# Kernel optimization log

Measured on AMD Instinct MI355X. Metric: run time of the kernel, lower is better.

## Reference

```python
import jax, jax.numpy as jnp
import numpy as np

B, N, F_IN = 256, 256, 128
HID, DEPTH = 48, 4
D_OUT = 97                 # sum(latent_dim [32,32,32,1]) = GraphUNet out_channels
K_SORT = 30
C1, C2, KW2 = 16, 32, 5
POOL_LEN = (K_SORT - 2) // 2 + 1        # 15 after maxpool1d(2,2)
DENSE_DIM = (POOL_LEN - KW2 + 1) * C2   # 352
OUT_DIM = 32


def _gcn(x, A, W, b):
    # GCNConv(improved=True): A_hat = A + 2I; out = D^-1/2 A_hat D^-1/2 (x W) + b
    n = A.shape[-1]
    Ah = A + 2.0 * jnp.eye(n, dtype=A.dtype)
    dinv = jax.lax.rsqrt(jnp.sum(Ah, axis=-1))          # deg >= 2 always
    An = dinv[:, :, None] * Ah * dinv[:, None, :]
    return An @ (x @ W) + b


def _augment(A):
    # GraphUNet.augment_adj: add self loops, two-hop (A@A), remove self loops
    n = A.shape[-1]
    eye = jnp.eye(n, dtype=A.dtype)
    A1 = A + eye
    return (A1 @ A1) * (1.0 - eye)


def _topk_pool(x, A, p):
    # TopKPooling(ratio=0.5, nonlinearity=tanh): score = tanh(x.p/||p||)
    Bb, n, _ = x.shape
    score = jnp.tanh((x @ p) / jnp.sqrt(jnp.sum(p * p)))
    k = (n + 1) // 2
    vals, perm = jax.lax.top_k(score, k)                # [B,k]
    bidx = jnp.arange(Bb)[:, None]
    xp = x[bidx, perm] * vals[..., None]                # gate kept nodes by score
    Ap = A[bidx[..., None], perm[:, :, None], perm[:, None, :]]
    return xp, Ap, perm


def _forward(x, A, dW0, db0, dW, db, pool_p, uW, ub, uWl, ubl, c1W, c1b, c2W, c2b, oW, ob):
    act = jax.nn.relu
    # ---- GraphUNet down path ----
    h = act(_gcn(x, A, dW0, db0))
    xs, As, perms = [h], [A], []
    Acur = A
    for i in range(DEPTH):
        A2 = _augment(Acur)
        h, Acur, perm = _topk_pool(h, A2, pool_p[i])
        h = act(_gcn(h, Acur, dW[i], db[i]))
        if i < DEPTH - 1:
            xs.append(h)
            As.append(Acur)
        perms.append(perm)
    # ---- up path with sum skip connections ----
    for i in range(DEPTH):
        j = DEPTH - 1 - i
        res, Aj, perm = xs[j], As[j], perms[j]
        bidx = jnp.arange(res.shape[0])[:, None]
        up = jnp.zeros_like(res).at[bidx, perm].set(h)
        h = res + up
        if i < DEPTH - 1:
            h = act(_gcn(h, Aj, uW[i], ub[i]))
        else:
            h = _gcn(h, Aj, uWl, ubl)                   # [B,N,D_OUT], no act
    # ---- global_sort_pool: sort nodes by last channel desc, keep top K_SORT ----
    _, order = jax.lax.top_k(h[..., -1], K_SORT)
    sp = h[jnp.arange(B)[:, None], order]               # [B,K_SORT,D_OUT]
    # conv1d(1->C1, kernel=stride=D_OUT) on flattened [B,1,K*D] == per-node linear
    y = jax.nn.relu(jnp.einsum('bkd,cd->bck', sp, c1W) + c1b[None, :, None])  # [B,C1,K]
    y = y.reshape(B, C1, POOL_LEN, 2).max(-1)           # maxpool1d(2,2)
    y = jax.lax.conv_general_dilated(y, c2W, (1,), 'VALID',
                                     dimension_numbers=('NCH', 'OIH', 'NCH'))
    y = jax.nn.relu(y + c2b[None, :, None])             # [B,C2,POOL_LEN-KW2+1]
    return jax.nn.relu(y.reshape(B, -1) @ oW + ob)      # relu(relu(.)) == relu(.)


def setup_inputs():
    key = jax.random.key(0)
    ks = jax.random.split(key, 12)
    x = jax.random.normal(ks[0], (B, N, F_IN), dtype=jnp.float32)
    # symmetric binary adjacency, no self loops, avg degree ~15
    u = jax.random.uniform(ks[1], (B, N, N))
    A = (u < 0.03).astype(jnp.float32)
    A = jnp.maximum(A, A.transpose(0, 2, 1)) * (1.0 - jnp.eye(N, dtype=jnp.float32))
    s = lambda f: np.float32(1.0 / np.sqrt(f))
    return dict(
        x=x, A=A,
        dW0=jax.random.normal(ks[2], (F_IN, HID), dtype=jnp.float32) * s(F_IN),
        db0=jnp.zeros((HID,), jnp.float32),
        dW=jax.random.normal(ks[3], (DEPTH, HID, HID), dtype=jnp.float32) * s(HID),
        db=jnp.zeros((DEPTH, HID), jnp.float32),
        pool_p=jax.random.normal(ks[4], (DEPTH, HID), dtype=jnp.float32) * s(HID),
        uW=jax.random.normal(ks[5], (DEPTH - 1, HID, HID), dtype=jnp.float32) * s(HID),
        ub=jnp.zeros((DEPTH - 1, HID), jnp.float32),
        uWl=jax.random.normal(ks[6], (HID, D_OUT), dtype=jnp.float32) * s(HID),
        ubl=jnp.zeros((D_OUT,), jnp.float32),
        c1W=jax.random.normal(ks[7], (C1, D_OUT), dtype=jnp.float32) * s(D_OUT),
        c1b=jnp.zeros((C1,), jnp.float32),
        c2W=jax.random.normal(ks[8], (C2, C1, KW2), dtype=jnp.float32) * s(C1 * KW2),
        c2b=jnp.zeros((C2,), jnp.float32),
        oW=jax.random.normal(ks[9], (DENSE_DIM, OUT_DIM), dtype=jnp.float32) * s(DENSE_DIM),
        ob=jnp.zeros((OUT_DIM,), jnp.float32),
    )


def reference(x, A, dW0, db0, dW, db, pool_p, uW, ub, uWl, ubl, c1W, c1b, c2W, c2b, oW, ob):
    return _forward(x, A, dW0, db0, dW, db, pool_p, uW, ub, uWl, ubl, c1W, c1b, c2W, c2b, oW, ob)
```

## Files before the change

### kernel.cpp

```cpp
#include <hip/hip_runtime.h>
#include <math.h>

#define BATCH 256
#define NNODE 256
#define FIN   128
#define HID   48
#define DOUT  97

#define WOFF_DW0 0
#define WOFF_DW  6144
#define WOFF_UW  18432
#define WOFF_UWL 27648
#define WTOT     34816

typedef __attribute__((ext_vector_type(8))) short bf16x8_t;
typedef __attribute__((ext_vector_type(4))) float f32x4_t;

__device__ inline unsigned short f2bf(float x) {
  unsigned u = __float_as_uint(x);
  u += 0x7fff + ((u >> 16) & 1);
  return (unsigned short)(u >> 16);
}
__device__ inline float bf2f(unsigned short h) {
  return __uint_as_float(((unsigned)h) << 16);
}

template<int L> __device__ inline float grp_sum(float v) {
  #pragma unroll
  for (int o = L >> 1; o > 0; o >>= 1) v += __shfl_xor(v, o);
  return v;
}
template<int L> __device__ inline int grp_isum(int v) {
  #pragma unroll
  for (int o = L >> 1; o > 0; o >>= 1) v += __shfl_xor(v, o);
  return v;
}

__global__ __launch_bounds__(256) void k_prepA(const float* __restrict__ A,
                                               unsigned short* __restrict__ Abf,
                                               float* __restrict__ dinv, int rows) {
  int wid = (blockIdx.x * 256 + threadIdx.x) >> 6;
  int lane = threadIdx.x & 63;
  if (wid >= rows) return;
  const float4* rp = (const float4*)(A + (size_t)wid * 256);
  float4 v = rp[lane];
  unsigned long long pk = (unsigned long long)f2bf(v.x)
                        | ((unsigned long long)f2bf(v.y) << 16)
                        | ((unsigned long long)f2bf(v.z) << 32)
                        | ((unsigned long long)f2bf(v.w) << 48);
  *(unsigned long long*)(Abf + (size_t)wid * 256 + lane * 4) = pk;
  float s = v.x + v.y + v.z + v.w;
  #pragma unroll
  for (int o = 32; o > 0; o >>= 1) s += __shfl_down(s, o);
  if (lane == 0) dinv[wid] = 1.0f / sqrtf(s + 2.0f);
}

__global__ __launch_bounds__(256) void k_splitW3(const float* __restrict__ dW0,
                                                 const float* __restrict__ dW,
                                                 const float* __restrict__ uW,
                                                 const float* __restrict__ uWl,
                                                 unsigned short* __restrict__ Wp) {
  int idx = blockIdx.x * 256 + threadIdx.x;
  if (idx >= WTOT) return;
  float v;
  if (idx < WOFF_DW) {
    int f = idx / 128, kk = idx - f * 128;
    v = dW0[kk * HID + f];
  } else if (idx < WOFF_UW) {
    int r = idx - WOFF_DW;
    int i = r / 3072; r -= i * 3072;
    int f = r / 64, kk = r - f * 64;
    v = (kk < HID) ? dW[((size_t)i * HID + kk) * HID + f] : 0.f;
  } else if (idx < WOFF_UWL) {
    int r = idx - WOFF_UW;
    int i = r / 3072; r -= i * 3072;
    int f = r / 64, kk = r - f * 64;
    v = (kk < HID) ? uW[((size_t)i * HID + kk) * HID + f] : 0.f;
  } else {
    int r = idx - WOFF_UWL;
    int f = r / 64, kk = r - f * 64;
    v = (f < DOUT && kk < HID) ? uWl[(size_t)kk * DOUT + f] : 0.f;
  }
  unsigned short h = f2bf(v);
  float r1 = v - bf2f(h);
  unsigned short m = f2bf(r1);
  float r2 = r1 - bf2f(m);
  unsigned short l = f2bf(r2);
  Wp[idx] = h;
  Wp[idx + WTOT] = m;
  Wp[idx + 2 * WTOT] = l;
}

template<int KS2>
__global__ __launch_bounds__(256) void k_xws(const float* __restrict__ X,
                                             const unsigned short* __restrict__ Wp,
                                             float* __restrict__ XW,
                                             const float* __restrict__ dinv,
                                             unsigned short* __restrict__ Yth,
                                             unsigned short* __restrict__ Ytl,
                                             int K, int F, int Fpad, int nShift) {
  constexpr int KP = KS2 * 32;
  int mt = (blockIdx.x * 256 + threadIdx.x) >> 6;
  int lane = threadIdx.x & 63;
  int r = lane & 15, q = lane >> 4;
  const float* xr = X + ((long)mt * 16 + r) * K;
  bf16x8_t ah[KS2], am[KS2], al[KS2];
  #pragma unroll
  for (int ks = 0; ks < KS2; ks++) {
    int col0 = ks * 32 + q * 8;
    float v[8];
    if (col0 + 8 <= K) {
      float4 a = *(const float4*)(xr + col0);
      float4 b = *(const float4*)(xr + col0 + 4);
      v[0] = a.x; v[1] = a.y; v[2] = a.z; v[3] = a.w;
      v[4] = b.x; v[5] = b.y; v[6] = b.z; v[7] = b.w;
    } else {
      #pragma unroll
      for (int j = 0; j < 8; j++) v[j] = (col0 + j < K) ? xr[col0 + j] : 0.f;
    }
    #pragma unroll
    for (int j = 0; j < 8; j++) {
      unsigned short h = f2bf(v[j]);
      float r1 = v[j] - bf2f(h);
      unsigned short m = f2bf(r1);
      float r2 = r1 - bf2f(m);
      unsigned short l = f2bf(r2);
      ah[ks][j] = (short)h;
      am[ks][j] = (short)m;
      al[ks][j] = (short)l;
    }
  }
  long row0 = (long)mt * 16 + q * 4;
  float4 dv4 = {0.f, 0.f, 0.f, 0.f};
  long ytBase = 0;
  if (Yth) {
    dv4 = *(const float4*)(dinv + row0);
    int bb = (int)(row0 >> nShift);
    int jj = (int)(row0 & ((1 << nShift) - 1));
    ytBase = (long)bb * Fpad;
    ytBase = ytBase << nShift;
    ytBase += jj;
  }
  int nFT = Fpad >> 4;
  for (int ft = 0; ft < nFT; ft++) {
    int fl = ft * 16 + r;
    const unsigned short* wb = Wp + (size_t)fl * KP + q * 8;
    f32x4_t acc = {0.f, 0.f, 0.f, 0.f};
    #pragma unroll
    for (int ks = 0; ks < KS2; ks++) {
      bf16x8_t bh = *(const bf16x8_t*)(wb + ks * 32);
      bf16x8_t bm = *(const bf16x8_t*)(wb + WTOT + ks * 32);
      bf16x8_t bl = *(const bf16x8_t*)(wb + 2 * WTOT + ks * 32);
      acc = __builtin_amdgcn_mfma_f32_16x16x32_bf16(ah[ks], bh, acc, 0, 0, 0);
      acc = __builtin_amdgcn_mfma_f32_16x16x32_bf16(ah[ks], bm, acc, 0, 0, 0);
      acc = __builtin_amdgcn_mfma_f32_16x16x32_bf16(am[ks], bh, acc, 0, 0, 0);
      acc = __builtin_amdgcn_mfma_f32_16x16x32_bf16(am[ks], bm, acc, 0, 0, 0);
      acc = __builtin_amdgcn_mfma_f32_16x16x32_bf16(ah[ks], bl, acc, 0, 0, 0);
      acc = __builtin_amdgcn_mfma_f32_16x16x32_bf16(al[ks], bh, acc, 0, 0, 0);
    }
    int f = fl;
    if (f < F) {
      if (XW) {
        #pragma unroll
        for (int reg = 0; reg < 4; reg++) XW[(row0 + reg) * F + f] = acc[reg];
      }
      if (Yth) {
        float dvv[4] = {dv4.x, dv4.y, dv4.z, dv4.w};
        unsigned long long hpk = 0, lpk = 0;
        #pragma unroll
        for (int reg = 0; reg < 4; reg++) {
          float v = dvv[reg] * acc[reg];
          unsigned short hi = f2bf(v);
          unsigned short lo = f2bf(v - bf2f(hi));
          hpk |= ((unsigned long long)hi) << (16 * reg);
          lpk |= ((unsigned long long)lo) << (16 * reg);
        }
        long o = ytBase + ((long)f << nShift);
        *(unsigned long long*)(Yth + o) = hpk;
        *(unsigned long long*)(Ytl + o) = lpk;
      }
    }
  }
}

__global__ __launch_bounds__(1024) void k_big(const float* __restrict__ x,
                                              const unsigned short* __restrict__ Wp0,
                                              const unsigned short* __restrict__ Abf0,
                                              const float* __restrict__ D0,
                                              const float* __restrict__ db0,
                                              float* __restrict__ H0) {
  __shared__ __align__(16) char yt0[24576];
  __shared__ __align__(16) char yt1[24576];
  int b = blockIdx.x, t = threadIdx.x;
  int w = t >> 6, lane = t & 63;
  int r = lane & 15, q = lane >> 4;
  const float* Xb = x + (size_t)b * 256 * 128;
  const float* Db = D0 + (size_t)b * 256;
  {
    int m = w;
    const float* xr = Xb + (size_t)(m * 16 + r) * 128;
    bf16x8_t ah[4], am[4], al[4];
    #pragma unroll
    for (int ks = 0; ks < 4; ks++) {
      int col0 = ks * 32 + q * 8;
      float4 a4 = *(const float4*)(xr + col0);
      float4 b4 = *(const float4*)(xr + col0 + 4);
      float v[8] = {a4.x, a4.y, a4.z, a4.w, b4.x, b4.y, b4.z, b4.w};
      #pragma unroll
      for (int j = 0; j < 8; j++) {
        unsigned short h = f2bf(v[j]); float r1 = v[j] - bf2f(h);
        unsigned short mm = f2bf(r1);  float r2 = r1 - bf2f(mm);
        ah[ks][j] = (short)h; am[ks][j] = (short)mm; al[ks][j] = (short)f2bf(r2);
      }
    }
    int row0 = m * 16 + q * 4;
    float4 dv4 = *(const float4*)(Db + row0);
    float dvv[4] = {dv4.x, dv4.y, dv4.z, dv4.w};
    #pragma unroll
    for (int ft = 0; ft < 3; ft++) {
      int fl = ft * 16 + r;
      const unsigned short* wb = Wp0 + (size_t)fl * 128 + q * 8;
      f32x4_t acc = {0.f, 0.f, 0.f, 0.f};
      #pragma unroll
      for (int ks = 0; ks < 4; ks++) {
        bf16x8_t bh = *(const bf16x8_t*)(wb + ks * 32);
        bf16x8_t bm = *(const bf16x8_t*)(wb + WTOT + ks * 32);
        bf16x8_t bl = *(const bf16x8_t*)(wb + 2 * WTOT + ks * 32);
        acc = __builtin_amdgcn_mfma_f32_16x16x32_bf16(ah[ks], bh, acc, 0, 0, 0);
        acc = __builtin_amdgcn_mfma_f32_16x16x32_bf16(ah[ks], bm, acc, 0, 0, 0);
        acc = __builtin_amdgcn_mfma_f32_16x16x32_bf16(am[ks], bh, acc, 0, 0, 0);
        acc = __builtin_amdgcn_mfma_f32_16x16x32_bf16(am[ks], bm, acc, 0, 0, 0);
        acc = __builtin_amdgcn_mfma_f32_16x16x32_bf16(ah[ks], bl, acc, 0, 0, 0);
        acc = __builtin_amdgcn_mfma_f32_16x16x32_bf16(al[ks], bh, acc, 0, 0, 0);
      }
      #pragma unroll
      for (int reg = 0; reg < 4; reg++) {
        float vv = dvv[reg] * acc[reg];
        unsigned short hi = f2bf(vv);
        unsigned short lo = f2bf(vv - bf2f(hi));
        int byte = (fl * 512 + (row0 + reg) * 2) ^ ((fl & 7) << 4);
        *(unsigned short*)(yt0 + byte) = hi;
        *(unsigned short*)(yt1 + byte) = lo;
      }
    }
  }
  __syncthreads();
  {
    int it = w;
    const unsigned short* ap = Abf0 + ((size_t)b * 256 + it * 16 + r) * 256 + q * 8;
    bf16x8_t af[8];
    #pragma unroll
    for (int ks = 0; ks < 8; ks++) af[ks] = *(const bf16x8_t*)(ap + ks * 32);
    #pragma unroll
    for (int ft = 0; ft < 3; ft++) {
      int fl = ft * 16 + r;
      f32x4_t acc = {0.f, 0.f, 0.f, 0.f};
      #pragma unroll
      for (int ks = 0; ks < 8; ks++) {
        int byte = (fl * 512 + (ks * 32 + q * 8) * 2) ^ ((fl & 7) << 4);
        bf16x8_t bh = *(const bf16x8_t*)(yt0 + byte);
        bf16x8_t bl = *(const bf16x8_t*)(yt1 + byte);
        acc = __builtin_amdgcn_mfma_f32_16x16x32_bf16(af[ks], bh, acc, 0, 0, 0);
        acc = __builtin_amdgcn_mfma_f32_16x16x32_bf16(af[ks], bl, acc, 0, 0, 0);
      }
      float bfv = db0[fl];
      #pragma unroll
      for (int reg = 0; reg < 4; reg++) {
        int rr = it * 16 + q * 4 + reg;
        int sbyte = (fl * 512 + rr * 2) ^ ((fl & 7) << 4);
        float selfv = bf2f(*(const unsigned short*)(yt0 + sbyte))
                    + bf2f(*(const unsigned short*)(yt1 + sbyte));
        float d = Db[rr];
        float v = d * acc[reg] + 2.f * d * selfv + bfv;
        H0[((size_t)b * 256 + rr) * 48 + fl] = fmaxf(v, 0.f);
      }
    }
  }
}

template<int MODE>
__device__ inline void gcn128_phase(const float* __restrict__ Xg,
                                    const unsigned short* __restrict__ Wpl,
                                    const unsigned short* __restrict__ A1,
                                    const float* __restrict__ D1b,
                                    const float* __restrict__ bias,
                                    char* yt0, char* yt1,
                                    float* __restrict__ H1,
                                    float* __restrict__ H0b,
                                    const int* sPerm1, int t) {
  int w = t >> 6, lane = t & 63;
  int r = lane & 15, q = lane >> 4;
  for (int task = w; task < 24; task += 16) {
    int m = task / 3, ft = task - m * 3;
    const float* xr = Xg + (size_t)(m * 16 + r) * 48;
    bf16x8_t ah[2], am[2], al[2];
    #pragma unroll
    for (int ks = 0; ks < 2; ks++) {
      int col0 = ks * 32 + q * 8;
      float v[8];
      if (col0 + 8 <= 48) {
        float4 a4 = *(const float4*)(xr + col0);
        float4 b4 = *(const float4*)(xr + col0 + 4);
        v[0]=a4.x; v[1]=a4.y; v[2]=a4.z; v[3]=a4.w;
        v[4]=b4.x; v[5]=b4.y; v[6]=b4.z; v[7]=b4.w;
      } else {
        #pragma unroll
        for (int j = 0; j < 8; j++) v[j] = (col0 + j < 48) ? xr[col0 + j] : 0.f;
      }
      #pragma unroll
      for (int j = 0; j < 8; j++) {
        unsigned short h = f2bf(v[j]); float r1 = v[j] - bf2f(h);
        unsigned short mm = f2bf(r1);  float r2 = r1 - bf2f(mm);
        ah[ks][j] = (short)h; am[ks][j] = (short)mm; al[ks][j] = (short)f2bf(r2);
      }
    }
    int row0 = m * 16 + q * 4;
    float4 dv4 = *(const float4*)(D1b + row0);
    float dvv[4] = {dv4.x, dv4.y, dv4.z, dv4.w};
    int fl = ft * 16 + r;
    const unsigned short* wb = Wpl + (size_t)fl * 64 + q * 8;
    f32x4_t acc = {0.f, 0.f, 0.f, 0.f};
    #pragma unroll
    for (int ks = 0; ks < 2; ks++) {
      bf16x8_t bh = *(const bf16x8_t*)(wb + ks * 32);
      bf16x8_t bm = *(const bf16x8_t*)(wb + WTOT + ks * 32);
      bf16x8_t bl = *(const bf16x8_t*)(wb + 2 * WTOT + ks * 32);
      acc = __builtin_amdgcn_mfma_f32_16x16x32_bf16(ah[ks], bh, acc, 0, 0, 0);
      acc = __builtin_amdgcn_mfma_f32_16x16x32_bf16(ah[ks], bm, acc, 0, 0, 0);
      acc = __builtin_amdgcn_mfma_f32_16x16x32_bf16(am[ks], bh, acc, 0, 0, 0);
      acc = __builtin_amdgcn_mfma_f32_16x16x32_bf16(am[ks], bm, acc, 0, 0, 0);
      acc = __builtin_amdgcn_mfma_f32_16x16x32_bf16(ah[ks], bl, acc, 0, 0, 0);
      acc = __builtin_amdgcn_mfma_f32_16x16x32_bf16(al[ks], bh, acc, 0, 0, 0);
    }
    #pragma unroll
    for (int reg = 0; reg < 4; reg++) {
      float vv = dvv[reg] * acc[reg];
      unsigned short hi = f2bf(vv);
      unsigned short lo = f2bf(vv - bf2f(hi));
      int byte = (fl * 256 + (row0 + reg) * 2) ^ ((fl & 7) << 4);
      *(unsigned short*)(yt0 + byte) = hi;
      *(unsigned short*)(yt1 + byte) = lo;
    }
  }
  __syncthreads();
  for (int task = w; task < 24; task += 16) {
    int it = task / 3, ft = task - it * 3;
    const unsigned short* ap = A1 + (size_t)(it * 16 + r) * 128 + q * 8;
    bf16x8_t af[4];
    #pragma unroll
    for (int ks = 0; ks < 4; ks++) af[ks] = *(const bf16x8_t*)(ap + ks * 32);
    int fl = ft * 16 + r;
    f32x4_t acc = {0.f, 0.f, 0.f, 0.f};
    #pragma unroll
    for (int ks = 0; ks < 4; ks++) {
      int byte = (fl * 256 + (ks * 32 + q * 8) * 2) ^ ((fl & 7) << 4);
      bf16x8_t bh = *(const bf16x8_t*)(yt0 + byte);
      bf16x8_t bl = *(const bf16x8_t*)(yt1 + byte);
      acc = __builtin_amdgcn_mfma_f32_16x16x32_bf16(af[ks], bh, acc, 0, 0, 0);
      acc = __builtin_amdgcn_mfma_f32_16x16x32_bf16(af[ks], bl, acc, 0, 0, 0);
    }
    float bfv = bias[fl];
    #pragma unroll
    for (int reg = 0; reg < 4; reg++) {
      int rr = it * 16 + q * 4 + reg;
      int sbyte = (fl * 256 + rr * 2) ^ ((fl & 7) << 4);
      float selfv = bf2f(*(const unsigned short*)(yt0 + sbyte))
                  + bf2f(*(const unsigned short*)(yt1 + sbyte));
      float d = D1b[rr];
      float v = d * acc[reg] + 2.f * d * selfv + bfv;
      v = fmaxf(v, 0.f);
      if (MODE == 0) H1[(size_t)rr * 48 + fl] = v;
      else {
        int node = sPerm1[rr];
        H0b[(size_t)node * 48 + fl] += v;
      }
    }
  }
  __syncthreads();
}

__device__ inline void xw_dphase(const float* hin, const float* W, const float* dv,
                                 float* xwd, int n, int t) {
  for (int idx = t; idx < n * 48; idx += 1024) {
    int j = idx / 48, f = idx - j * 48;
    const float* hr = hin + j * 48;
    float a = 0.f;
    #pragma unroll
    for (int g = 0; g < 48; g++) a += hr[g] * W[g * 48 + f];
    xwd[idx] = dv[j] * a;
  }
}

__device__ inline void anxw_phase(const float* A, int lda, const float* xwd,
                                  const float* dv, const float* bias,
                                  float* hout, int n, int t) {
  for (int idx = t; idx < n * 48; idx += 1024) {
    int i = idx / 48, f = idx - i * 48;
    const float* ar = A + i * lda;
    float acc = 0.f;
    #pragma unroll 4
    for (int j = 0; j < n; j++) acc += ar[j] * xwd[j * 48 + f];
    float di = dv[i];
    float v = di * acc + 2.f * di * xwd[i * 48 + f] + bias[f];
    hout[idx] = fmaxf(v, 0.f);
  }
}

template<int N, int K>
__device__ inline void pool_phaseT(const float* h, const float* p,
                                   float* sS, int* perm, float* hin, int t) {
  constexpr int LPR = 1024 / N;
  int row = t / LPR, sub = t % LPR;
  float pn = 0.f;
  #pragma unroll
  for (int g = 0; g < 48; g++) pn += p[g] * p[g];
  const float* hr = h + row * 48;
  float acc = 0.f;
  for (int g = sub; g < 48; g += LPR) acc += hr[g] * p[g];
  acc = grp_sum<LPR>(acc);
  if (sub == 0) sS[row] = tanhf(acc / sqrtf(pn));
  __syncthreads();
  {
    float v = sS[row];
    int r = 0;
    for (int j = sub; j < N; j += LPR) {
      float u = sS[j];
      r += (u > v) || (u == v && j < row);
    }
    r = grp_isum<LPR>(r);
    if (sub == 0 && r < K) perm[r] = row;
  }
  __syncthreads();
  for (int idx = t; idx < K * 48; idx += 1024) {
    int r = idx / 48, g = idx - r * 48;
    int pi = perm[r];
    hin[idx] = h[pi * 48 + g] * sS[pi];
  }
  __syncthreads();
}

template<int NN, int KK>
__device__ inline void aug_phaseT(const float* A, int lda, const int* perm,
                                  float* Ao, int ldo, float* dout, int t) {
  for (int idx = t; idx < KK * KK; idx += 1024) {
    int r = idx / KK, c = idx - r * KK;
    int pr = perm[r], pc = perm[c];
    const float* ra = A + pr * lda;
    const float* rc = A + pc * lda;
    float acc = 0.f;
    #pragma unroll 4
    for (int j = 0; j < NN; j++) acc += ra[j] * rc[j];
    float v = acc + 2.f * ra[pc];
    Ao[r * ldo + c] = (r == c) ? 0.f : v;
  }
  __syncthreads();
  {
    constexpr int LPR = 1024 / KK;
    int row = t / LPR, sub = t % LPR;
    float s = 0.f;
    for (int j = sub; j < KK; j += LPR) s += Ao[row * ldo + j];
    s = grp_sum<(LPR > 64 ? 64 : LPR)>(s);
    if (sub == 0) dout[row] = 1.0f / sqrtf(s + 2.0f);
  }
  __syncthreads();
}

__device__ inline void scat_phase(const int* perm, const float* src, float* dst,
                                  int k, int t) {
  for (int idx = t; idx < k * 48; idx += 1024) {
    int r = idx / 48, g = idx - r * 48;
    dst[perm[r] * 48 + g] += src[idx];
  }
  __syncthreads();
}

__global__ __launch_bounds__(1024) void k_mid(const unsigned short* __restrict__ Abf0,
                                              unsigned short* __restrict__ Abf1g,
                                              float* __restrict__ H0,
                                              float* __restrict__ H1g,
                                              float* __restrict__ D1g,
                                              const unsigned short* __restrict__ Wp,
                                              const float* __restrict__ dW,
                                              const float* __restrict__ dbv,
                                              const float* __restrict__ pp,
                                              const float* __restrict__ uW,
                                              const float* __restrict__ ub) {
  int b = blockIdx.x, t = threadIdx.x;
  __shared__ __align__(16) char arena[63488];
  __shared__ int sPerm1[128];
  float* H1 = H1g + (size_t)b * 128 * 48;
  float* H0b = H0 + (size_t)b * 256 * 48;
  unsigned short* A1 = Abf1g + (size_t)b * 128 * 128;
  float* D1b = D1g + (size_t)b * 128;

  {
    float* sc = (float*)arena;
    const float* p = pp;
    float pn = 0.f;
    #pragma unroll
    for (int g = 0; g < 48; g++) pn += p[g] * p[g];
    int row = t >> 2, sub = t & 3;
    const float* hr = H0b + (size_t)row * 48;
    float a = 0.f;
    for (int g = sub; g < 48; g += 4) a += hr[g] * p[g];
    a = grp_sum<4>(a);
    if (!sub) sc[row] = tanhf(a / sqrtf(pn));
    __syncthreads();
    float vv = sc[row];
    int rk = 0;
    for (int j = sub; j < 256; j += 4) {
      float u = sc[j];
      rk += (u > vv) || (u == vv && j < row);
    }
    rk = grp_isum<4>(rk);
    if (!sub && rk < 128) sPerm1[rk] = row;
    __syncthreads();
    for (int idx = t; idx < 128 * 48; idx += 1024) {
      int rr = idx / 48, g = idx - rr * 48;
      int pi = sPerm1[rr];
      H1[idx] = H0b[(size_t)pi * 48 + g] * sc[pi];
    }
  }
  __syncthreads();

  {
    int w = t >> 6, lane = t & 63;
    int r = lane & 15, q = lane >> 4;
    int it = w >> 1, fh = w & 1;
    int rowA = sPerm1[it * 16 + r];
    const unsigned short* Ab = Abf0 + (size_t)b * 256 * 256;
    const unsigned short* pa = Ab + (size_t)rowA * 256 + q * 8;
    bf16x8_t af[8];
    #pragma unroll
    for (int ks = 0; ks < 8; ks++) {
      bf16x8_t a = *(const bf16x8_t*)(pa + ks * 32);
      int da = rowA - ks * 32 - q * 8;
      #pragma unroll
      for (int e = 0; e < 8; e++) if (da == e) a[e] = (short)0x3F80;
      af[ks] = a;
    }
    for (int ft = fh * 4; ft < fh * 4 + 4; ft++) {
      int rowB = sPerm1[ft * 16 + r];
      const unsigned short* pb = Ab + (size_t)rowB * 256 + q * 8;
      f32x4_t acc = {0.f, 0.f, 0.f, 0.f};
      #pragma unroll
      for (int ks = 0; ks < 8; ks++) {
        bf16x8_t bv = *(const bf16x8_t*)(pb + ks * 32);
        int db_ = rowB - ks * 32 - q * 8;
        #pragma unroll
        for (int e = 0; e < 8; e++) if (db_ == e) bv[e] = (short)0x3F80;
        acc = __builtin_amdgcn_mfma_f32_16x16x32_bf16(af[ks], bv, acc, 0, 0, 0);
      }
      int c = ft * 16 + r;
      #pragma unroll
      for (int reg = 0; reg < 4; reg++) {
        int rr = it * 16 + q * 4 + reg;
        float v = (rr == c) ? 0.f : acc[reg];
        A1[(size_t)rr * 128 + c] = f2bf(v);
      }
    }
  }
  __syncthreads();
  {
    int row = t >> 3, sub = t & 7;
    const unsigned* ar = (const unsigned*)(A1 + (size_t)row * 128);
    float s = 0.f;
    for (int jj = sub; jj < 64; jj += 8) {
      unsigned u = ar[jj];
      s += bf2f((unsigned short)(u & 0xffffu)) + bf2f((unsigned short)(u >> 16));
    }
    s = grp_sum<8>(s);
    if (sub == 0) D1b[row] = 1.0f / sqrtf(s + 2.0f);
  }
  __syncthreads();

  gcn128_phase<0>(H1, Wp + WOFF_DW, A1, D1b, dbv,
                  (char*)arena, (char*)arena + 12288, H1, nullptr, sPerm1, t);

  {
    float* sS  = (float*)(arena);
    int*   sP2 = (int*)(arena + 512);
    int*   sP3 = (int*)(arena + 768);
    int*   sP4 = (int*)(arena + 896);
    float* sD2 = (float*)(arena + 960);
    float* sD3 = (float*)(arena + 1216);
    float* sD4 = (float*)(arena + 1344);
    float* sA2 = (float*)(arena + 1536);
    float* sA3 = (float*)(arena + 18176);
    float* sH2 = (float*)(arena + 22400);
    float* sH3 = (float*)(arena + 34688);
    float* sXW = (float*)(arena + 40832);
    float* hin = (float*)(arena + 53120);
    float* sH4 = (float*)(arena + 59264);
    float* sA4 = (float*)(arena + 62336);

    {
      const float* p = pp + 48;
      float pn = 0.f;
      #pragma unroll
      for (int g = 0; g < 48; g++) pn += p[g] * p[g];
      int row = t >> 3, sub = t & 7;
      const float* hr = H1 + (size_t)row * 48;
      float acc = 0.f;
      for (int g = sub; g < 48; g += 8) acc += hr[g] * p[g];
      acc = grp_sum<8>(acc);
      if (sub == 0) sS[row] = tanhf(acc / sqrtf(pn));
      __syncthreads();
      float v = sS[row];
      int rk = 0;
      for (int j = sub; j < 128; j += 8) {
        float u = sS[j];
        rk += (u > v) || (u == v && j < row);
      }
      rk = grp_isum<8>(rk);
      if (sub == 0 && rk < 64) sP2[rk] = row;
      __syncthreads();
    }
    {
      int w = t >> 6, lane = t & 63;
      int r = lane & 15, q = lane >> 4;
      int it = w >> 2, ft = w & 3;
      int rowA = sP2[it * 16 + r];
      int rowB = sP2[ft * 16 + r];
      const unsigned short* pa = A1 + (size_t)rowA * 128 + q * 8;
      const unsigned short* pb = A1 + (size_t)rowB * 128 + q * 8;
      f32x4_t acc = {0.f, 0.f, 0.f, 0.f};
      #pragma unroll
      for (int k0 = 0; k0 < 128; k0 += 32) {
        bf16x8_t a  = *(const bf16x8_t*)(pa + k0);
        bf16x8_t bv = *(const bf16x8_t*)(pb + k0);
        int daA = rowA - k0 - q * 8;
        int daB = rowB - k0 - q * 8;
        #pragma unroll
        for (int e = 0; e < 8; e++) {
          if (daA == e) a[e] = (short)0x3F80;
          if (daB == e) bv[e] = (short)0x3F80;
        }
        acc = __builtin_amdgcn_mfma_f32_16x16x32_bf16(a, bv, acc, 0, 0, 0);
      }
      int c = ft * 16 + r;
      #pragma unroll
      for (int reg = 0; reg < 4; reg++) {
        int rr = it * 16 + q * 4 + reg;
        sA2[rr * 65 + c] = (rr == c) ? 0.f : acc[reg];
      }
    }
    __syncthreads();
    {
      int row = t >> 4, sub = t & 15;
      float s = 0.f;
      for (int j = sub; j < 64; j += 16) s += sA2[row * 65 + j];
      s = grp_sum<16>(s);
      if (sub == 0) sD2[row] = 1.0f / sqrtf(s + 2.0f);
    }
    __syncthreads();
    for (int idx = t; idx < 64 * 48; idx += 1024) {
      int j = idx / 48, f = idx - j * 48;
      int pi = sP2[j];
      const float* hr = H1 + (size_t)pi * 48;
      const float* W = dW + 2304;
      float a = 0.f;
      #pragma unroll
      for (int g = 0; g < 48; g++) a += hr[g] * W[g * 48 + f];
      sXW[idx] = sD2[j] * sS[pi] * a;
    }
    __syncthreads();
    anxw_phase(sA2, 65, sXW, sD2, dbv + 48, sH2, 64, t);
    __syncthreads();

    pool_phaseT<64, 32>(sH2, pp + 96, sS, sP3, hin, t);
    aug_phaseT<64, 32>(sA2, 65, sP3, sA3, 33, sD3, t);
    xw_dphase(hin, dW + 2 * 2304, sD3, sXW, 32, t);
    __syncthreads();
    anxw_phase(sA3, 33, sXW, sD3, dbv + 96, sH3, 32, t);
    __syncthreads();

    pool_phaseT<32, 16>(sH3, pp + 144, sS, sP4, hin, t);
    aug_phaseT<32, 16>(sA3, 33, sP4, sA4, 17, sD4, t);
    xw_dphase(hin, dW + 3 * 2304, sD4, sXW, 16, t);
    __syncthreads();
    anxw_phase(sA4, 17, sXW, sD4, dbv + 144, sH4, 16, t);
    __syncthreads();

    scat_phase(sP4, sH4, sH3, 16, t);
    xw_dphase(sH3, uW, sD3, sXW, 32, t);
    __syncthreads();
    anxw_phase(sA3, 33, sXW, sD3, ub, sH3, 32, t);
    __syncthreads();

    scat_phase(sP3, sH3, sH2, 32, t);
    xw_dphase(sH2, uW + 2304, sD2, sXW, 64, t);
    __syncthreads();
    anxw_phase(sA2, 65, sXW, sD2, ub + 48, sH2, 64, t);
    __syncthreads();

    for (int idx = t; idx < 64 * 48; idx += 1024) {
      int r2 = idx / 48, g = idx - r2 * 48;
      H1[(size_t)sP2[r2] * 48 + g] += sH2[idx];
    }
  }
  __syncthreads();

  gcn128_phase<1>(H1, Wp + WOFF_UW + 2 * 3072, A1, D1b, ub + 96,
                  (char*)arena, (char*)arena + 12288, nullptr, H0b, sPerm1, t);
}

__global__ __launch_bounds__(1024) void k_htail(const unsigned short* __restrict__ Abf,
                                                const float* __restrict__ dinv,
                                                const unsigned short* __restrict__ Yth,
                                                const unsigned short* __restrict__ Ytl,
                                                const float* __restrict__ ubl,
                                                float* __restrict__ sp) {
  int b = blockIdx.x, t = threadIdx.x;
  __shared__ float sy[256];
  __shared__ float sc[256];
  __shared__ int sord[32];
  const unsigned short* yh = Yth + ((size_t)b * 112 + 96) * 256;
  const unsigned short* yl = Ytl + ((size_t)b * 112 + 96) * 256;
  if (t < 256) sy[t] = bf2f(yh[t]) + bf2f(yl[t]);
  __syncthreads();
  {
    int i = t >> 2, sub = t & 3;
    const unsigned short* ar = Abf + ((size_t)b * 256 + i) * 256 + sub * 64;
    const float* syp = sy + sub * 64;
    float s = 0.f;
    for (int j = 0; j < 64; j += 2) {
      unsigned u = *(const unsigned*)(ar + j);
      s += bf2f((unsigned short)(u & 0xffffu)) * syp[j]
         + bf2f((unsigned short)(u >> 16)) * syp[j + 1];
    }
    s = grp_sum<4>(s);
    if (sub == 0) {
      float d = dinv[(size_t)b * 256 + i];
      sc[i] = d * s + 2.f * d * sy[i];
    }
  }
  __syncthreads();
  {
    int i = t >> 2, sub = t & 3;
    float v = sc[i];
    int rk = 0;
    int j0 = sub * 64;
    for (int j = j0; j < j0 + 64; j++) {
      float u = sc[j];
      rk += (u > v) || (u == v && j < i);
    }
    rk = grp_isum<4>(rk);
    if (sub == 0 && rk < 30) sord[rk] = i;
  }
  __syncthreads();
  int w = t >> 6, lane = t & 63;
  if (w < 14) {
    int it = w / 7, ft = w % 7;
    int r = lane & 15, q = lane >> 4;
    int ari = it * 16 + r;
    int arow = sord[ari < 30 ? ari : 0];
    const unsigned short* ap = Abf + ((size_t)b * 256 + arow) * 256 + q * 8;
    bf16x8_t af[8];
    #pragma unroll
    for (int ks = 0; ks < 8; ks++) af[ks] = *(const bf16x8_t*)(ap + ks * 32);
    int fl = ft * 16 + r;
    const unsigned short* yrowh = Yth + ((size_t)b * 112 + fl) * 256;
    const unsigned short* yrowl = Ytl + ((size_t)b * 112 + fl) * 256;
    f32x4_t acc = {0.f, 0.f, 0.f, 0.f};
    #pragma unroll
    for (int ks = 0; ks < 8; ks++) {
      bf16x8_t bh = *(const bf16x8_t*)(yrowh + q * 8 + ks * 32);
      bf16x8_t bl = *(const bf16x8_t*)(yrowl + q * 8 + ks * 32);
      acc = __builtin_amdgcn_mfma_f32_16x16x32_bf16(af[ks], bh, acc, 0, 0, 0);
      acc = __builtin_amdgcn_mfma_f32_16x16x32_bf16(af[ks], bl, acc, 0, 0, 0);
    }
    if (fl < DOUT) {
      float bf = ubl[fl];
      #pragma unroll
      for (int reg = 0; reg < 4; reg++) {
        int rowidx = it * 16 + q * 4 + reg;
        if (rowidx < 30) {
          int node = sord[rowidx];
          float d = dinv[(size_t)b * 256 + node];
          float yv = bf2f(yrowh[node]) + bf2f(yrowl[node]);
          sp[((size_t)b * 30 + rowidx) * DOUT + fl] = d * acc[reg] + 2.f * d * yv + bf;
        }
      }
    }
  }
}

__global__ __launch_bounds__(256) void k_head2(const float* __restrict__ spg,
                                               const float* __restrict__ c1W,
                                               const float* __restrict__ c1b,
                                               const float* __restrict__ c2W,
                                               const float* __restrict__ c2b,
                                               const float* __restrict__ oW,
                                               const float* __restrict__ ob,
                                               float* __restrict__ out) {
  int b = blockIdx.x, t = threadIdx.x;
  __shared__ float sp[30 * 97];
  __shared__ float y1[16 * 30];
  __shared__ float yp[16 * 15];
  __shared__ float yc[32 * 11];
  __shared__ float red[256];
  const float* spb = spg + (size_t)b * 30 * 97;
  for (int idx = t; idx < 30 * 97; idx += 256) sp[idx] = spb[idx];
  __syncthreads();
  for (int idx = t; idx < 16 * 30; idx += 256) {
    int c = idx / 30, kk = idx - c * 30;
    float a = c1b[c];
    for (int d = 0; d < 97; d++) a += sp[kk * 97 + d] * c1W[c * 97 + d];
    y1[c * 30 + kk] = fmaxf(a, 0.f);
  }
  __syncthreads();
  for (int idx = t; idx < 16 * 15; idx += 256) {
    int c = idx / 15, t2 = idx - c * 15;
    yp[idx] = fmaxf(y1[c * 30 + 2 * t2], y1[c * 30 + 2 * t2 + 1]);
  }
  __syncthreads();
  for (int idx = t; idx < 32 * 11; idx += 256) {
    int o = idx / 11, t3 = idx - o * 11;
    float a = c2b[o];
    for (int i2 = 0; i2 < 16; i2++)
      for (int w = 0; w < 5; w++)
        a += yp[i2 * 15 + t3 + w] * c2W[(o * 16 + i2) * 5 + w];
    yc[o * 11 + t3] = fmaxf(a, 0.f);
  }
  __syncthreads();
  {
    int o = t & 31, g = t >> 5;
    float a = 0.f;
    for (int qq = g * 44; qq < g * 44 + 44; qq++) a += yc[qq] * oW[qq * 32 + o];
    red[t] = a;
  }
  __syncthreads();
  if (t < 32) {
    float a = ob[t];
    #pragma unroll
    for (int g = 0; g < 8; g++) a += red[t + 32 * g];
    out[(size_t)b * 32 + t] = fmaxf(a, 0.f);
  }
}

extern "C" void kernel_launch(void* const* d_in, const int* in_sizes, int n_in,
                              void* d_out, int out_size, void* d_ws, size_t ws_size,
                              hipStream_t stream) {
  const float* x   = (const float*)d_in[0];
  const float* A0  = (const float*)d_in[1];
  const float* dW0 = (const float*)d_in[2];
  const float* db0 = (const float*)d_in[3];
  const float* dW  = (const float*)d_in[4];
  const float* dbv = (const float*)d_in[5];
  const float* pp  = (const float*)d_in[6];
  const float* uW  = (const float*)d_in[7];
  const float* ub  = (const float*)d_in[8];
  const float* uWl = (const float*)d_in[9];
  const float* ubl = (const float*)d_in[10];
  const float* c1W = (const float*)d_in[11];
  const float* c1b = (const float*)d_in[12];
  const float* c2W = (const float*)d_in[13];
  const float* c2b = (const float*)d_in[14];
  const float* oW  = (const float*)d_in[15];
  const float* ob  = (const float*)d_in[16];
  float* out = (float*)d_out;

  float* base = (float*)d_ws;
  size_t off = 0;
  auto alloc = [&](size_t nel) { nel = (nel + 3) & ~(size_t)3; float* p = base + off; off += nel; return p; };
  float* H0 = alloc((size_t)BATCH * 256 * HID);
  float* H1 = alloc((size_t)BATCH * 128 * HID);
  float* D0 = alloc((size_t)BATCH * 256);
  float* D1 = alloc((size_t)BATCH * 128);
  float* SP = alloc((size_t)BATCH * 30 * 97);
  unsigned short* Abf0 = (unsigned short*)alloc((size_t)BATCH * 256 * 256 / 2);
  unsigned short* Abf1 = (unsigned short*)alloc((size_t)BATCH * 128 * 128 / 2);
  unsigned short* Yth  = (unsigned short*)alloc((size_t)BATCH * 112 * 256 / 2);
  unsigned short* Ytl  = (unsigned short*)alloc((size_t)BATCH * 112 * 256 / 2);
  unsigned short* Wp   = (unsigned short*)alloc((size_t)3 * WTOT / 2 + 4);

  k_prepA<<<BATCH * 256 / 4, 256, 0, stream>>>(A0, Abf0, D0, BATCH * 256);
  k_splitW3<<<(WTOT + 255) / 256, 256, 0, stream>>>(dW0, dW, uW, uWl, Wp);

  k_big<<<BATCH, 1024, 0, stream>>>(x, Wp + WOFF_DW0, Abf0, D0, db0, H0);

  k_mid<<<BATCH, 1024, 0, stream>>>(Abf0, Abf1, H0, H1, D1, Wp, dW, dbv, pp, uW, ub);

  k_xws<2><<<BATCH * 256 / 64, 256, 0, stream>>>(H0, Wp + WOFF_UWL, nullptr,
                                                 D0, Yth, Ytl, HID, DOUT, 112, 8);
  k_htail<<<BATCH, 1024, 0, stream>>>(Abf0, D0, Yth, Ytl, ubl, SP);

  k_head2<<<BATCH, 256, 0, stream>>>(SP, c1W, c1b, c2W, c2b, oW, ob, out);
}
```

Baseline: 356.0 us.

## Fuse final XW projection into tail kernel and merge pool/augment phases

```diff
diff --git a/kernel.cpp b/kernel.cpp
--- a/kernel.cpp
+++ b/kernel.cpp
@@ -91,98 +91,6 @@
   Wp[idx + 2 * WTOT] = l;
 }
 
-template<int KS2>
-__global__ __launch_bounds__(256) void k_xws(const float* __restrict__ X,
-                                             const unsigned short* __restrict__ Wp,
-                                             float* __restrict__ XW,
-                                             const float* __restrict__ dinv,
-                                             unsigned short* __restrict__ Yth,
-                                             unsigned short* __restrict__ Ytl,
-                                             int K, int F, int Fpad, int nShift) {
-  constexpr int KP = KS2 * 32;
-  int mt = (blockIdx.x * 256 + threadIdx.x) >> 6;
-  int lane = threadIdx.x & 63;
-  int r = lane & 15, q = lane >> 4;
-  const float* xr = X + ((long)mt * 16 + r) * K;
-  bf16x8_t ah[KS2], am[KS2], al[KS2];
-  #pragma unroll
-  for (int ks = 0; ks < KS2; ks++) {
-    int col0 = ks * 32 + q * 8;
-    float v[8];
-    if (col0 + 8 <= K) {
-      float4 a = *(const float4*)(xr + col0);
-      float4 b = *(const float4*)(xr + col0 + 4);
-      v[0] = a.x; v[1] = a.y; v[2] = a.z; v[3] = a.w;
-      v[4] = b.x; v[5] = b.y; v[6] = b.z; v[7] = b.w;
-    } else {
-      #pragma unroll
-      for (int j = 0; j < 8; j++) v[j] = (col0 + j < K) ? xr[col0 + j] : 0.f;
-    }
-    #pragma unroll
-    for (int j = 0; j < 8; j++) {
-      unsigned short h = f2bf(v[j]);
-      float r1 = v[j] - bf2f(h);
-      unsigned short m = f2bf(r1);
-      float r2 = r1 - bf2f(m);
-      unsigned short l = f2bf(r2);
-      ah[ks][j] = (short)h;
-      am[ks][j] = (short)m;
-      al[ks][j] = (short)l;
-    }
-  }
-  long row0 = (long)mt * 16 + q * 4;
-  float4 dv4 = {0.f, 0.f, 0.f, 0.f};
-  long ytBase = 0;
-  if (Yth) {
-    dv4 = *(const float4*)(dinv + row0);
-    int bb = (int)(row0 >> nShift);
-    int jj = (int)(row0 & ((1 << nShift) - 1));
-    ytBase = (long)bb * Fpad;
-    ytBase = ytBase << nShift;
-    ytBase += jj;
-  }
-  int nFT = Fpad >> 4;
-  for (int ft = 0; ft < nFT; ft++) {
-    int fl = ft * 16 + r;
-    const unsigned short* wb = Wp + (size_t)fl * KP + q * 8;
-    f32x4_t acc = {0.f, 0.f, 0.f, 0.f};
-    #pragma unroll
-    for (int ks = 0; ks < KS2; ks++) {
-      bf16x8_t bh = *(const bf16x8_t*)(wb + ks * 32);
-      bf16x8_t bm = *(const bf16x8_t*)(wb + WTOT + ks * 32);
-      bf16x8_t bl = *(const bf16x8_t*)(wb + 2 * WTOT + ks * 32);
-      acc = __builtin_amdgcn_mfma_f32_16x16x32_bf16(ah[ks], bh, acc, 0, 0, 0);
-      acc = __builtin_amdgcn_mfma_f32_16x16x32_bf16(ah[ks], bm, acc, 0, 0, 0);
-      acc = __builtin_amdgcn_mfma_f32_16x16x32_bf16(am[ks], bh, acc, 0, 0, 0);
-      acc = __builtin_amdgcn_mfma_f32_16x16x32_bf16(am[ks], bm, acc, 0, 0, 0);
-      acc = __builtin_amdgcn_mfma_f32_16x16x32_bf16(ah[ks], bl, acc, 0, 0, 0);
-      acc = __builtin_amdgcn_mfma_f32_16x16x32_bf16(al[ks], bh, acc, 0, 0, 0);
-    }
-    int f = fl;
-    if (f < F) {
-      if (XW) {
-        #pragma unroll
-        for (int reg = 0; reg < 4; reg++) XW[(row0 + reg) * F + f] = acc[reg];
-      }
-      if (Yth) {
-        float dvv[4] = {dv4.x, dv4.y, dv4.z, dv4.w};
-        unsigned long long hpk = 0, lpk = 0;
-        #pragma unroll
-        for (int reg = 0; reg < 4; reg++) {
-          float v = dvv[reg] * acc[reg];
-          unsigned short hi = f2bf(v);
-          unsigned short lo = f2bf(v - bf2f(hi));
-          hpk |= ((unsigned long long)hi) << (16 * reg);
-          lpk |= ((unsigned long long)lo) << (16 * reg);
-        }
-        long o = ytBase + ((long)f << nShift);
-        *(unsigned long long*)(Yth + o) = hpk;
-        *(unsigned long long*)(Ytl + o) = lpk;
-      }
-    }
-  }
-}
-
 __global__ __launch_bounds__(1024) void k_big(const float* __restrict__ x,
                                               const unsigned short* __restrict__ Wp0,
                                               const unsigned short* __restrict__ Abf0,
@@ -407,8 +315,11 @@
 }
 
 template<int N, int K>
-__device__ inline void pool_phaseT(const float* h, const float* p,
-                                   float* sS, int* perm, float* hin, int t) {
+__device__ inline void pool_aug_phaseT(const float* h, const float* p,
+                                       const float* A, int lda,
+                                       float* Ao, int ldo,
+                                       float* sS, int* perm, float* hin,
+                                       float* dout, int t) {
   constexpr int LPR = 1024 / N;
   int row = t / LPR, sub = t % LPR;
   float pn = 0.f;
@@ -422,13 +333,13 @@
   __syncthreads();
   {
     float v = sS[row];
-    int r = 0;
+    int rk = 0;
     for (int j = sub; j < N; j += LPR) {
       float u = sS[j];
-      r += (u > v) || (u == v && j < row);
-    }
-    r = grp_isum<LPR>(r);
-    if (sub == 0 && r < K) perm[r] = row;
+      rk += (u > v) || (u == v && j < row);
+    }
+    rk = grp_isum<LPR>(rk);
+    if (sub == 0 && rk < K) perm[rk] = row;
   }
   __syncthreads();
   for (int idx = t; idx < K * 48; idx += 1024) {
@@ -436,31 +347,26 @@
     int pi = perm[r];
     hin[idx] = h[pi * 48 + g] * sS[pi];
   }
-  __syncthreads();
-}
-
-template<int NN, int KK>
-__device__ inline void aug_phaseT(const float* A, int lda, const int* perm,
-                                  float* Ao, int ldo, float* dout, int t) {
-  for (int idx = t; idx < KK * KK; idx += 1024) {
-    int r = idx / KK, c = idx - r * KK;
+  for (int idx = t; idx < K * K; idx += 1024) {
+    int r = idx / K, c = idx - r * K;
     int pr = perm[r], pc = perm[c];
     const float* ra = A + pr * lda;
     const float* rc = A + pc * lda;
-    float acc = 0.f;
+    float a2 = 0.f;
     #pragma unroll 4
-    for (int j = 0; j < NN; j++) acc += ra[j] * rc[j];
-    float v = acc + 2.f * ra[pc];
+    for (int j = 0; j < N; j++) a2 += ra[j] * rc[j];
+    float v = a2 + 2.f * ra[pc];
     Ao[r * ldo + c] = (r == c) ? 0.f : v;
   }
   __syncthreads();
   {
-    constexpr int LPR = 1024 / KK;
-    int row = t / LPR, sub = t % LPR;
+    constexpr int LPR2 = 1024 / K;
+    constexpr int LG = (LPR2 > 64 ? 64 : LPR2);
+    int row2 = t / LPR2, sub2 = t % LPR2;
     float s = 0.f;
-    for (int j = sub; j < KK; j += LPR) s += Ao[row * ldo + j];
-    s = grp_sum<(LPR > 64 ? 64 : LPR)>(s);
-    if (sub == 0) dout[row] = 1.0f / sqrtf(s + 2.0f);
+    for (int j = sub2; j < K; j += LPR2) s += Ao[row2 * ldo + j];
+    s = grp_sum<LG>(s);
+    if (sub2 == 0) dout[row2] = 1.0f / sqrtf(s + 2.0f);
   }
   __syncthreads();
 }
@@ -514,16 +420,16 @@
     }
     rk = grp_isum<4>(rk);
     if (!sub && rk < 128) sPerm1[rk] = row;
-    __syncthreads();
+  }
+  __syncthreads();
+
+  {
+    float* sc = (float*)arena;
     for (int idx = t; idx < 128 * 48; idx += 1024) {
       int rr = idx / 48, g = idx - rr * 48;
       int pi = sPerm1[rr];
       H1[idx] = H0b[(size_t)pi * 48 + g] * sc[pi];
     }
-  }
-  __syncthreads();
-
-  {
     int w = t >> 6, lane = t & 63;
     int r = lane & 15, q = lane >> 4;
     int it = w >> 1, fh = w & 1;
@@ -668,15 +574,13 @@
     anxw_phase(sA2, 65, sXW, sD2, dbv + 48, sH2, 64, t);
     __syncthreads();
 
-    pool_phaseT<64, 32>(sH2, pp + 96, sS, sP3, hin, t);
-    aug_phaseT<64, 32>(sA2, 65, sP3, sA3, 33, sD3, t);
+    pool_aug_phaseT<64, 32>(sH2, pp + 96, sA2, 65, sA3, 33, sS, sP3, hin, sD3, t);
     xw_dphase(hin, dW + 2 * 2304, sD3, sXW, 32, t);
     __syncthreads();
     anxw_phase(sA3, 33, sXW, sD3, dbv + 96, sH3, 32, t);
     __syncthreads();
 
-    pool_phaseT<32, 16>(sH3, pp + 144, sS, sP4, hin, t);
-    aug_phaseT<32, 16>(sA3, 33, sP4, sA4, 17, sD4, t);
+    pool_aug_phaseT<32, 16>(sH3, pp + 144, sA3, 33, sA4, 17, sS, sP4, hin, sD4, t);
     xw_dphase(hin, dW + 3 * 2304, sD4, sXW, 16, t);
     __syncthreads();
     anxw_phase(sA4, 17, sXW, sD4, dbv + 144, sH4, 16, t);
@@ -705,34 +609,108 @@
                   (char*)arena, (char*)arena + 12288, nullptr, H0b, sPerm1, t);
 }
 
-__global__ __launch_bounds__(1024) void k_htail(const unsigned short* __restrict__ Abf,
-                                                const float* __restrict__ dinv,
-                                                const unsigned short* __restrict__ Yth,
-                                                const unsigned short* __restrict__ Ytl,
-                                                const float* __restrict__ ubl,
-                                                float* __restrict__ sp) {
+__global__ __launch_bounds__(1024) void k_tail(const float* __restrict__ H0,
+                                               const unsigned short* __restrict__ Wpl,
+                                               const unsigned short* __restrict__ Abf,
+                                               const float* __restrict__ dinv,
+                                               const float* __restrict__ ubl,
+                                               float* __restrict__ sp) {
   int b = blockIdx.x, t = threadIdx.x;
-  __shared__ float sy[256];
+  __shared__ float ydt[16][257];
   __shared__ float sc[256];
   __shared__ int sord[32];
-  const unsigned short* yh = Yth + ((size_t)b * 112 + 96) * 256;
-  const unsigned short* yl = Ytl + ((size_t)b * 112 + 96) * 256;
-  if (t < 256) sy[t] = bf2f(yh[t]) + bf2f(yl[t]);
+  int w = t >> 6, lane = t & 63;
+  int r = lane & 15, q = lane >> 4;
+  const float* H0b = H0 + (size_t)b * 256 * 48;
+  const float* Db = dinv + (size_t)b * 256;
+
+  bf16x8_t ah[2], am[2], al[2];
+  {
+    const float* xr = H0b + (size_t)(w * 16 + r) * 48;
+    #pragma unroll
+    for (int ks = 0; ks < 2; ks++) {
+      int col0 = ks * 32 + q * 8;
+      float v[8];
+      if (col0 + 8 <= 48) {
+        float4 a4 = *(const float4*)(xr + col0);
+        float4 b4 = *(const float4*)(xr + col0 + 4);
+        v[0]=a4.x; v[1]=a4.y; v[2]=a4.z; v[3]=a4.w;
+        v[4]=b4.x; v[5]=b4.y; v[6]=b4.z; v[7]=b4.w;
+      } else {
+        #pragma unroll
+        for (int j = 0; j < 8; j++) v[j] = (col0 + j < 48) ? xr[col0 + j] : 0.f;
+      }
+      #pragma unroll
+      for (int j = 0; j < 8; j++) {
+        unsigned short h = f2bf(v[j]); float r1 = v[j] - bf2f(h);
+        unsigned short mm = f2bf(r1);  float r2 = r1 - bf2f(mm);
+        ah[ks][j] = (short)h; am[ks][j] = (short)mm; al[ks][j] = (short)f2bf(r2);
+      }
+    }
+  }
+  int row0 = w * 16 + q * 4;
+  float4 dv4 = *(const float4*)(Db + row0);
+  float dvv[4] = {dv4.x, dv4.y, dv4.z, dv4.w};
+
+  auto stepA = [&](int ft) {
+    int fl = ft * 16 + r;
+    const unsigned short* wb = Wpl + (size_t)fl * 64 + q * 8;
+    f32x4_t acc = {0.f, 0.f, 0.f, 0.f};
+    #pragma unroll
+    for (int ks = 0; ks < 2; ks++) {
+      bf16x8_t bh = *(const bf16x8_t*)(wb + ks * 32);
+      bf16x8_t bm = *(const bf16x8_t*)(wb + WTOT + ks * 32);
+      bf16x8_t bl = *(const bf16x8_t*)(wb + 2 * WTOT + ks * 32);
+      acc = __builtin_amdgcn_mfma_f32_16x16x32_bf16(ah[ks], bh, acc, 0, 0, 0);
+      acc = __builtin_amdgcn_mfma_f32_16x16x32_bf16(ah[ks], bm, acc, 0, 0, 0);
+      acc = __builtin_amdgcn_mfma_f32_16x16x32_bf16(am[ks], bh, acc, 0, 0, 0);
+      acc = __builtin_amdgcn_mfma_f32_16x16x32_bf16(am[ks], bm, acc, 0, 0, 0);
+      acc = __builtin_amdgcn_mfma_f32_16x16x32_bf16(ah[ks], bl, acc, 0, 0, 0);
+      acc = __builtin_amdgcn_mfma_f32_16x16x32_bf16(al[ks], bh, acc, 0, 0, 0);
+    }
+    #pragma unroll
+    for (int reg = 0; reg < 4; reg++)
+      ydt[r][row0 + reg] = dvv[reg] * acc[reg];
+  };
+
+  auto stepB = [&](int ft, int nf) {
+    int o = t >> 1, sub = t & 1;
+    if (o < 30 * nf) {
+      int rr = o / nf, f = o - rr * nf;
+      int fl = ft * 16 + f;
+      int node = sord[rr];
+      const unsigned short* ar = Abf + ((size_t)b * 256 + node) * 256 + sub * 128;
+      const float* yp = &ydt[f][sub * 128];
+      float s = 0.f;
+      for (int j = 0; j < 128; j += 2) {
+        unsigned u = *(const unsigned*)(ar + j);
+        s += bf2f((unsigned short)(u & 0xffffu)) * yp[j]
+           + bf2f((unsigned short)(u >> 16)) * yp[j + 1];
+      }
+      s += __shfl_xor(s, 1);
+      if (!sub) {
+        float d = Db[node];
+        sp[((size_t)b * 30 + rr) * DOUT + fl] = d * s + 2.f * d * ydt[f][node] + ubl[fl];
+      }
+    }
+  };
+
+  stepA(6);
   __syncthreads();
   {
     int i = t >> 2, sub = t & 3;
     const unsigned short* ar = Abf + ((size_t)b * 256 + i) * 256 + sub * 64;
-    const float* syp = sy + sub * 64;
+    const float* yp = &ydt[0][sub * 64];
     float s = 0.f;
     for (int j = 0; j < 64; j += 2) {
       unsigned u = *(const unsigned*)(ar + j);
-      s += bf2f((unsigned short)(u & 0xffffu)) * syp[j]
-         + bf2f((unsigned short)(u >> 16)) * syp[j + 1];
+      s += bf2f((unsigned short)(u & 0xffffu)) * yp[j]
+         + bf2f((unsigned short)(u >> 16)) * yp[j + 1];
     }
     s = grp_sum<4>(s);
-    if (sub == 0) {
-      float d = dinv[(size_t)b * 256 + i];
-      sc[i] = d * s + 2.f * d * sy[i];
+    if (!sub) {
+      float d = Db[i];
+      sc[i] = d * s + 2.f * d * ydt[0][i];
     }
   }
   __syncthreads();
@@ -746,43 +724,16 @@
       rk += (u > v) || (u == v && j < i);
     }
     rk = grp_isum<4>(rk);
-    if (sub == 0 && rk < 30) sord[rk] = i;
-  }
-  __syncthreads();
-  int w = t >> 6, lane = t & 63;
-  if (w < 14) {
-    int it = w / 7, ft = w % 7;
-    int r = lane & 15, q = lane >> 4;
-    int ari = it * 16 + r;
-    int arow = sord[ari < 30 ? ari : 0];
-    const unsigned short* ap = Abf + ((size_t)b * 256 + arow) * 256 + q * 8;
-    bf16x8_t af[8];
-    #pragma unroll
-    for (int ks = 0; ks < 8; ks++) af[ks] = *(const bf16x8_t*)(ap + ks * 32);
-    int fl = ft * 16 + r;
-    const unsigned short* yrowh = Yth + ((size_t)b * 112 + fl) * 256;
-    const unsigned short* yrowl = Ytl + ((size_t)b * 112 + fl) * 256;
-    f32x4_t acc = {0.f, 0.f, 0.f, 0.f};
-    #pragma unroll
-    for (int ks = 0; ks < 8; ks++) {
-      bf16x8_t bh = *(const bf16x8_t*)(yrowh + q * 8 + ks * 32);
-      bf16x8_t bl = *(const bf16x8_t*)(yrowl + q * 8 + ks * 32);
-      acc = __builtin_amdgcn_mfma_f32_16x16x32_bf16(af[ks], bh, acc, 0, 0, 0);
-      acc = __builtin_amdgcn_mfma_f32_16x16x32_bf16(af[ks], bl, acc, 0, 0, 0);
-    }
-    if (fl < DOUT) {
-      float bf = ubl[fl];
-      #pragma unroll
-      for (int reg = 0; reg < 4; reg++) {
-        int rowidx = it * 16 + q * 4 + reg;
-        if (rowidx < 30) {
-          int node = sord[rowidx];
-          float d = dinv[(size_t)b * 256 + node];
-          float yv = bf2f(yrowh[node]) + bf2f(yrowl[node]);
-          sp[((size_t)b * 30 + rowidx) * DOUT + fl] = d * acc[reg] + 2.f * d * yv + bf;
-        }
-      }
-    }
+    if (!sub && rk < 30) sord[rk] = i;
+  }
+  __syncthreads();
+  stepB(6, 1);
+  __syncthreads();
+  for (int ft = 0; ft < 6; ft++) {
+    stepA(ft);
+    __syncthreads();
+    stepB(ft, 16);
+    __syncthreads();
   }
 }
 
@@ -871,8 +822,6 @@
   float* SP = alloc((size_t)BATCH * 30 * 97);
   unsigned short* Abf0 = (unsigned short*)alloc((size_t)BATCH * 256 * 256 / 2);
   unsigned short* Abf1 = (unsigned short*)alloc((size_t)BATCH * 128 * 128 / 2);
-  unsigned short* Yth  = (unsigned short*)alloc((size_t)BATCH * 112 * 256 / 2);
-  unsigned short* Ytl  = (unsigned short*)alloc((size_t)BATCH * 112 * 256 / 2);
   unsigned short* Wp   = (unsigned short*)alloc((size_t)3 * WTOT / 2 + 4);
 
   k_prepA<<<BATCH * 256 / 4, 256, 0, stream>>>(A0, Abf0, D0, BATCH * 256);
@@ -882,9 +831,7 @@
 
   k_mid<<<BATCH, 1024, 0, stream>>>(Abf0, Abf1, H0, H1, D1, Wp, dW, dbv, pp, uW, ub);
 
-  k_xws<2><<<BATCH * 256 / 64, 256, 0, stream>>>(H0, Wp + WOFF_UWL, nullptr,
-                                                 D0, Yth, Ytl, HID, DOUT, 112, 8);
-  k_htail<<<BATCH, 1024, 0, stream>>>(Abf0, D0, Yth, Ytl, ubl, SP);
+  k_tail<<<BATCH, 1024, 0, stream>>>(H0, Wp + WOFF_UWL, Abf0, D0, ubl, SP);
 
   k_head2<<<BATCH, 256, 0, stream>>>(SP, c1W, c1b, c2W, c2b, oW, ob, out);
 }
```

After: 360.5 us. About the same (+1.2%).
